# Kernel tuning notes

Measured on AMD Instinct MI355X. Metric: run time of the kernel, lower is better.

## Reference

```python
import jax, jax.numpy as jnp
import numpy as np

EPS = 1e-07


def _splat_single(frame, flow):
    # frame: [C, H, W], flow: [2, H, W] -> bilinear forward splatting (summation)
    C, H, W = frame.shape
    gx = jnp.arange(W, dtype=frame.dtype)[None, :]   # [1, W]
    gy = jnp.arange(H, dtype=frame.dtype)[:, None]   # [H, 1]
    tx = gx + flow[0]                                 # [H, W]
    ty = gy + flow[1]
    fx = jnp.floor(tx)
    fy = jnp.floor(ty)
    dx = tx - fx
    dy = ty - fy
    fx = fx.astype(jnp.int32)
    fy = fy.astype(jnp.int32)

    src = frame.reshape(C, H * W)                     # [C, HW]
    out = jnp.zeros((C, H * W), dtype=frame.dtype)
    # four bilinear corners: (x, y, weight)
    corners = [
        (fx,     fy,     (1.0 - dx) * (1.0 - dy)),
        (fx + 1, fy,     dx * (1.0 - dy)),
        (fx,     fy + 1, (1.0 - dx) * dy),
        (fx + 1, fy + 1, dx * dy),
    ]
    for cx, cy, w in corners:
        valid = (cx >= 0) & (cx < W) & (cy >= 0) & (cy < H)
        idx = jnp.where(valid, cy * W + cx, 0).reshape(-1)          # [HW]
        wv = jnp.where(valid, w, 0.0).reshape(1, -1)                # [1, HW]
        out = out.at[:, idx].add(src * wv)
    return out.reshape(C, H, W)


def _softmax_splat(frame, flow, importance_metric, eps=EPS):
    imp = jnp.exp(importance_metric)                  # [B,1,H,W]
    aug = jnp.concatenate([frame * imp, imp], axis=1) # [B,C+1,H,W]
    out = jax.vmap(_splat_single)(aug, flow)          # [B,C+1,H,W]
    return out[:, :-1] / (out[:, -1:] + eps)


def setup_inputs() -> dict:
    key = jax.random.key(0)
    k1, k2, k3 = jax.random.split(key, 3)
    B, C, H, W = 8, 4, 512, 960
    frame = jax.random.normal(k1, (B, C, H, W), dtype=jnp.float32)
    flow = jax.random.normal(k2, (B, 2, H, W), dtype=jnp.float32)
    importance_metric = jax.random.normal(k3, (B, 1, H, W), dtype=jnp.float32)
    return {"frame": frame, "flow": flow, "importance_metric": importance_metric}


def reference(frame, flow, importance_metric):
    return _softmax_splat(frame, flow, importance_metric)
```

## Files before the change

### kernel.cpp

```cpp
#include <hip/hip_runtime.h>
#include <hip/hip_fp16.h>
#include <math.h>


#define EPS 1e-7f

constexpr int B = 8, C = 4, H = 512, W = 960;
constexpr int HW = H * W;
constexpr int CHW = C * HW;
constexpr int NPIX = B * HW;

constexpr int TX = 32, TY = 32;
constexpr int RAD = 3;
constexpr int GROWS = 38;
constexpr int QX = 10;
constexpr int NQUAD = QX * GROWS;
constexpr int LSTRIDE = 41;
constexpr int NCELL = GROWS * LSTRIDE;

constexpr int NTILE_X = W / TX;
constexpr int NTILE = NTILE_X * (H / TY);
constexpr int BUCKET_CAP = 64;

struct alignas(8) HPack { __half2 a; __half2 b; };

__global__ __launch_bounds__(256) void outlier_pass(
    const float* __restrict__ frame,
    const float* __restrict__ flow,
    const float* __restrict__ imp,
    int* __restrict__ bcnt,
    float* __restrict__ bucket)
{
    int idx = blockIdx.x * blockDim.x + threadIdx.x;
    if (idx >= NPIX) return;
    int b = idx / HW;
    int p = idx - b * HW;
    int sy = p / W;
    int sx = p - sy * W;

    const size_t flb = (size_t)b * 2 * HW;
    float flx = flow[flb + p];
    float fly = flow[flb + HW + p];

    if (fabsf(flx) <= (float)(RAD - 1) && fabsf(fly) <= (float)(RAD - 1)) return;

    float tx = (float)sx + flx;
    float ty = (float)sy + fly;
    float fxf = floorf(tx);
    float fyf = floorf(ty);
    float dx = tx - fxf;
    float dy = ty - fyf;
    int fx = (int)fxf;
    int fy = (int)fyf;

    const size_t fb = (size_t)b * CHW;
    float im = __expf(imp[(size_t)b * HW + p]);
    float f0 = frame[fb + 0 * HW + p] * im;
    float f1 = frame[fb + 1 * HW + p] * im;
    float f2 = frame[fb + 2 * HW + p] * im;
    float f3 = frame[fb + 3 * HW + p] * im;

    #pragma unroll
    for (int cyi = 0; cyi < 2; ++cyi) {
        #pragma unroll
        for (int cxi = 0; cxi < 2; ++cxi) {
            int cx = fx + cxi;
            int cy = fy + cyi;
            if ((unsigned)cx >= (unsigned)W || (unsigned)cy >= (unsigned)H) continue;
            int ax = cx - sx; if (ax < 0) ax = -ax;
            int ay = cy - sy; if (ay < 0) ay = -ay;
            if (ax <= RAD && ay <= RAD) continue;
            float w = (cxi ? dx : 1.0f - dx) * (cyi ? dy : 1.0f - dy);
            int tile = b * NTILE + (cy >> 5) * NTILE_X + (cx >> 5);
            int e = atomicAdd(&bcnt[tile], 1);
            if (e < BUCKET_CAP) {
                float* ent = bucket + ((size_t)tile * BUCKET_CAP + e) * 8;
                ent[0] = __int_as_float((cy & 31) * TX + (cx & 31));
                ent[1] = f0 * w;
                ent[2] = f1 * w;
                ent[3] = f2 * w;
                ent[4] = f3 * w;
                ent[5] = im * w;
            }
        }
    }
}

__global__ __launch_bounds__(256) void splat_gather(
    const float* __restrict__ frame,
    const float* __restrict__ flow,
    const float* __restrict__ imp,
    float* __restrict__ out,
    const int* __restrict__ bcnt,
    const float* __restrict__ bucket)
{
    __shared__ float smem[5 * NCELL];
    float2* XY = (float2*)smem;
    float*  IM = smem + 2 * NCELL;
    HPack*  CH = (HPack*)(smem + 3 * NCELL);

    const int tid = threadIdx.x;
    const int x0 = blockIdx.x * TX;
    const int y0 = blockIdx.y * TY;
    const int b  = blockIdx.z;

    const float* fxp   = flow + (size_t)b * 2 * HW;
    const float* fyp   = fxp + HW;
    const float* imp_p = imp + (size_t)b * HW;
    const float* c0p   = frame + (size_t)b * CHW;
    const float* c1p   = c0p + HW;
    const float* c2p   = c1p + HW;
    const float* c3p   = c2p + HW;

    #pragma unroll
    for (int it = 0; it < 2; ++it) {
        int q = tid + it * 256;
        if (q < NQUAD) {
            int r = q / QX;
            int c = q - r * QX;
            int sy = y0 - RAD + r;
            int sx0 = x0 - 4 + 4 * c;
            int p = sy * W + sx0;
            int pc = p < 0 ? 0 : (p > HW - 4 ? HW - 4 : p);
            bool qv = ((unsigned)sy < (unsigned)H) & ((unsigned)sx0 < (unsigned)W);

            float4 vfx = *(const float4*)(fxp + pc);
            float4 vfy = *(const float4*)(fyp + pc);
            float4 vim = *(const float4*)(imp_p + pc);
            float4 v0  = *(const float4*)(c0p + pc);
            float4 v1  = *(const float4*)(c1p + pc);
            float4 v2  = *(const float4*)(c2p + pc);
            float4 v3  = *(const float4*)(c3p + pc);

            float aflx[4] = {vfx.x, vfx.y, vfx.z, vfx.w};
            float afly[4] = {vfy.x, vfy.y, vfy.z, vfy.w};
            float aim [4] = {vim.x, vim.y, vim.z, vim.w};
            float a0  [4] = {v0.x,  v0.y,  v0.z,  v0.w};
            float a1  [4] = {v1.x,  v1.y,  v1.z,  v1.w};
            float a2  [4] = {v2.x,  v2.y,  v2.z,  v2.w};
            float a3  [4] = {v3.x,  v3.y,  v3.z,  v3.w};

            int base = r * LSTRIDE + c * 4;
            #pragma unroll
            for (int k = 0; k < 4; ++k) {
                float im = qv ? __expf(aim[k]) : 0.0f;
                float txv = (float)(sx0 + k) + aflx[k];
                float tyv = (float)sy + afly[k];
                XY[base + k] = make_float2(txv, tyv);
                IM[base + k] = im;
                HPack hp;
                hp.a = __floats2half2_rn(a0[k] * im, a1[k] * im);
                hp.b = __floats2half2_rn(a2[k] * im, a3[k] * im);
                CH[base + k] = hp;
            }
        }
    }
    __syncthreads();

    const int oy    = tid & 31;
    const int strip = tid >> 5;
    const int oxl   = strip * 4;
    const float oxf0 = (float)(x0 + oxl);
    const float oyf  = (float)(y0 + oy);

    float accw[4] = {0.f, 0.f, 0.f, 0.f};
    float acc0[4] = {0.f, 0.f, 0.f, 0.f};
    float acc1[4] = {0.f, 0.f, 0.f, 0.f};
    float acc2[4] = {0.f, 0.f, 0.f, 0.f};
    float acc3[4] = {0.f, 0.f, 0.f, 0.f};

    for (int dyi = 0; dyi < 2 * RAD + 1; ++dyi) {
        int rowoff = (oy + dyi) * LSTRIDE + oxl;
        #pragma unroll
        for (int dxi = 1; dxi <= 10; ++dxi) {
            float2 xy = XY[rowoff + dxi];
            float wy = fmaxf(0.0f, 1.0f - fabsf(xy.y - oyf));
            if (wy > 0.0f) {
                float d0  = xy.x - oxf0;
                float wx0 = (dxi <= 7)              ? fmaxf(0.0f, 1.0f - fabsf(d0))        : 0.0f;
                float wx1 = (dxi >= 2 && dxi <= 8)  ? fmaxf(0.0f, 1.0f - fabsf(d0 - 1.0f)) : 0.0f;
                float wx2 = (dxi >= 3 && dxi <= 9)  ? fmaxf(0.0f, 1.0f - fabsf(d0 - 2.0f)) : 0.0f;
                float wx3 = (dxi >= 4)              ? fmaxf(0.0f, 1.0f - fabsf(d0 - 3.0f)) : 0.0f;
                float t0 = wx0 * wy, t1 = wx1 * wy, t2 = wx2 * wy, t3 = wx3 * wy;
                if ((t0 + t1) + (t2 + t3) > 0.0f) {
                    float im = IM[rowoff + dxi];
                    accw[0] = fmaf(im, t0, accw[0]);
                    accw[1] = fmaf(im, t1, accw[1]);
                    accw[2] = fmaf(im, t2, accw[2]);
                    accw[3] = fmaf(im, t3, accw[3]);
                    HPack hp = CH[rowoff + dxi];
                    float2 f01 = __half22float2(hp.a);
                    float2 f23 = __half22float2(hp.b);
                    acc0[0] = fmaf(f01.x, t0, acc0[0]);
                    acc0[1] = fmaf(f01.x, t1, acc0[1]);
                    acc0[2] = fmaf(f01.x, t2, acc0[2]);
                    acc0[3] = fmaf(f01.x, t3, acc0[3]);
                    acc1[0] = fmaf(f01.y, t0, acc1[0]);
                    acc1[1] = fmaf(f01.y, t1, acc1[1]);
                    acc1[2] = fmaf(f01.y, t2, acc1[2]);
                    acc1[3] = fmaf(f01.y, t3, acc1[3]);
                    acc2[0] = fmaf(f23.x, t0, acc2[0]);
                    acc2[1] = fmaf(f23.x, t1, acc2[1]);
                    acc2[2] = fmaf(f23.x, t2, acc2[2]);
                    acc2[3] = fmaf(f23.x, t3, acc2[3]);
                    acc3[0] = fmaf(f23.y, t0, acc3[0]);
                    acc3[1] = fmaf(f23.y, t1, acc3[1]);
                    acc3[2] = fmaf(f23.y, t2, acc3[2]);
                    acc3[3] = fmaf(f23.y, t3, acc3[3]);
                }
            }
        }
    }

    __syncthreads();
    const int tile = b * NTILE + blockIdx.y * NTILE_X + blockIdx.x;
    int cnt = bcnt[tile];
    if (cnt > BUCKET_CAP) cnt = BUCKET_CAP;
    if (cnt > 0) {
        float* oacc = smem;
        for (int i = tid; i < 5 * 1024; i += 256) oacc[i] = 0.0f;
        __syncthreads();
        const float* bb = bucket + (size_t)tile * BUCKET_CAP * 8;
        for (int e = tid; e < cnt; e += 256) {
            const float* ent = bb + (size_t)e * 8;
            int cell = __float_as_int(ent[0]);
            atomicAdd(&oacc[0 * 1024 + cell], ent[1]);
            atomicAdd(&oacc[1 * 1024 + cell], ent[2]);
            atomicAdd(&oacc[2 * 1024 + cell], ent[3]);
            atomicAdd(&oacc[3 * 1024 + cell], ent[4]);
            atomicAdd(&oacc[4 * 1024 + cell], ent[5]);
        }
        __syncthreads();
        int cell0 = oy * TX + oxl;
        #pragma unroll
        for (int j = 0; j < 4; ++j) {
            acc0[j] += oacc[0 * 1024 + cell0 + j];
            acc1[j] += oacc[1 * 1024 + cell0 + j];
            acc2[j] += oacc[2 * 1024 + cell0 + j];
            acc3[j] += oacc[3 * 1024 + cell0 + j];
            accw[j] += oacc[4 * 1024 + cell0 + j];
        }
    }

    float o0[4], o1[4], o2[4], o3[4];
    #pragma unroll
    for (int j = 0; j < 4; ++j) {
        float inv = 1.0f / (accw[j] + EPS);
        o0[j] = acc0[j] * inv;
        o1[j] = acc1[j] * inv;
        o2[j] = acc2[j] * inv;
        o3[j] = acc3[j] * inv;
    }
    size_t obase = (size_t)b * CHW + (size_t)(y0 + oy) * W + (x0 + oxl);
    *(float4*)(out + obase + 0 * HW) = make_float4(o0[0], o0[1], o0[2], o0[3]);
    *(float4*)(out + obase + 1 * HW) = make_float4(o1[0], o1[1], o1[2], o1[3]);
    *(float4*)(out + obase + 2 * HW) = make_float4(o2[0], o2[1], o2[2], o2[3]);
    *(float4*)(out + obase + 3 * HW) = make_float4(o3[0], o3[1], o3[2], o3[3]);
}

extern "C" void kernel_launch(void* const* d_in, const int* in_sizes, int n_in,
                              void* d_out, int out_size, void* d_ws, size_t ws_size,
                              hipStream_t stream) {
    const float* frame = (const float*)d_in[0];
    const float* flow  = (const float*)d_in[1];
    const float* imp   = (const float*)d_in[2];
    float* out = (float*)d_out;

    int*   bcnt   = (int*)d_ws;
    float* bucket = (float*)((char*)d_ws + 16384);

    hipMemsetAsync(bcnt, 0, B * NTILE * sizeof(int), stream);

    outlier_pass<<<(NPIX + 255) / 256, 256, 0, stream>>>(frame, flow, imp, bcnt, bucket);

    dim3 grid(W / TX, H / TY, B);
    splat_gather<<<grid, 256, 0, stream>>>(frame, flow, imp, out, bcnt, bucket);
}
```

Baseline: 117.8 us.

## Use 2x2 output quads in gather and vectorize outlier pass over four pixels

The gather kernel now has each thread own a 2x2 block of output pixels instead of a 1x4 strip. That shrinks the source window it scans from 7x10 to 8x8 candidates and computes two y-weights and two x-weights per candidate. The outlier pass processes four pixels per thread with float4 flow loads, cutting thread count and making its loads wider. Together these aim to reduce shared-memory reads and weight arithmetic in the hot gather loop. In exchange, output stores narrow from float4 to float2, and the outlier pass may see more branch divergence.

```diff
diff --git a/kernel.cpp b/kernel.cpp
--- a/kernel.cpp
+++ b/kernel.cpp
@@ -31,56 +31,69 @@
     int* __restrict__ bcnt,
     float* __restrict__ bucket)
 {
-    int idx = blockIdx.x * blockDim.x + threadIdx.x;
-    if (idx >= NPIX) return;
-    int b = idx / HW;
-    int p = idx - b * HW;
-    int sy = p / W;
-    int sx = p - sy * W;
+    int g = blockIdx.x * blockDim.x + threadIdx.x;
+    if (g >= NPIX / 4) return;
+    const int QHW = HW / 4;
+    int b = g / QHW;
+    int q = g - b * QHW;
+    int p0 = q * 4;
+    int sy = p0 / W;
+    int sx0 = p0 - sy * W;
 
     const size_t flb = (size_t)b * 2 * HW;
-    float flx = flow[flb + p];
-    float fly = flow[flb + HW + p];
-
-    if (fabsf(flx) <= (float)(RAD - 1) && fabsf(fly) <= (float)(RAD - 1)) return;
-
-    float tx = (float)sx + flx;
-    float ty = (float)sy + fly;
-    float fxf = floorf(tx);
-    float fyf = floorf(ty);
-    float dx = tx - fxf;
-    float dy = ty - fyf;
-    int fx = (int)fxf;
-    int fy = (int)fyf;
+    float4 vfx = *(const float4*)(flow + flb + p0);
+    float4 vfy = *(const float4*)(flow + flb + HW + p0);
+    float aflx[4] = {vfx.x, vfx.y, vfx.z, vfx.w};
+    float afly[4] = {vfy.x, vfy.y, vfy.z, vfy.w};
 
     const size_t fb = (size_t)b * CHW;
-    float im = __expf(imp[(size_t)b * HW + p]);
-    float f0 = frame[fb + 0 * HW + p] * im;
-    float f1 = frame[fb + 1 * HW + p] * im;
-    float f2 = frame[fb + 2 * HW + p] * im;
-    float f3 = frame[fb + 3 * HW + p] * im;
-
-    #pragma unroll
-    for (int cyi = 0; cyi < 2; ++cyi) {
+    const size_t ib = (size_t)b * HW;
+
+    #pragma unroll
+    for (int k = 0; k < 4; ++k) {
+        float flx = aflx[k];
+        float fly = afly[k];
+        if (fabsf(flx) <= (float)(RAD - 1) && fabsf(fly) <= (float)(RAD - 1)) continue;
+
+        int sx = sx0 + k;
+        int p = p0 + k;
+        float tx = (float)sx + flx;
+        float ty = (float)sy + fly;
+        float fxf = floorf(tx);
+        float fyf = floorf(ty);
+        float dx = tx - fxf;
+        float dy = ty - fyf;
+        int fx = (int)fxf;
+        int fy = (int)fyf;
+
+        float im = __expf(imp[ib + p]);
+        float f0 = frame[fb + 0 * HW + p] * im;
+        float f1 = frame[fb + 1 * HW + p] * im;
+        float f2 = frame[fb + 2 * HW + p] * im;
+        float f3 = frame[fb + 3 * HW + p] * im;
+
         #pragma unroll
-        for (int cxi = 0; cxi < 2; ++cxi) {
-            int cx = fx + cxi;
-            int cy = fy + cyi;
-            if ((unsigned)cx >= (unsigned)W || (unsigned)cy >= (unsigned)H) continue;
-            int ax = cx - sx; if (ax < 0) ax = -ax;
-            int ay = cy - sy; if (ay < 0) ay = -ay;
-            if (ax <= RAD && ay <= RAD) continue;
-            float w = (cxi ? dx : 1.0f - dx) * (cyi ? dy : 1.0f - dy);
-            int tile = b * NTILE + (cy >> 5) * NTILE_X + (cx >> 5);
-            int e = atomicAdd(&bcnt[tile], 1);
-            if (e < BUCKET_CAP) {
-                float* ent = bucket + ((size_t)tile * BUCKET_CAP + e) * 8;
-                ent[0] = __int_as_float((cy & 31) * TX + (cx & 31));
-                ent[1] = f0 * w;
-                ent[2] = f1 * w;
-                ent[3] = f2 * w;
-                ent[4] = f3 * w;
-                ent[5] = im * w;
+        for (int cyi = 0; cyi < 2; ++cyi) {
+            #pragma unroll
+            for (int cxi = 0; cxi < 2; ++cxi) {
+                int cx = fx + cxi;
+                int cy = fy + cyi;
+                if ((unsigned)cx >= (unsigned)W || (unsigned)cy >= (unsigned)H) continue;
+                int ax = cx - sx; if (ax < 0) ax = -ax;
+                int ay = cy - sy; if (ay < 0) ay = -ay;
+                if (ax <= RAD && ay <= RAD) continue;
+                float w = (cxi ? dx : 1.0f - dx) * (cyi ? dy : 1.0f - dy);
+                int tile = b * NTILE + (cy >> 5) * NTILE_X + (cx >> 5);
+                int e = atomicAdd(&bcnt[tile], 1);
+                if (e < BUCKET_CAP) {
+                    float* ent = bucket + ((size_t)tile * BUCKET_CAP + e) * 8;
+                    ent[0] = __int_as_float((cy & 31) * TX + (cx & 31));
+                    ent[1] = f0 * w;
+                    ent[2] = f1 * w;
+                    ent[3] = f2 * w;
+                    ent[4] = f3 * w;
+                    ent[5] = im * w;
+                }
             }
         }
     }
@@ -157,11 +170,10 @@
     }
     __syncthreads();
 
-    const int oy    = tid & 31;
-    const int strip = tid >> 5;
-    const int oxl   = strip * 4;
-    const float oxf0 = (float)(x0 + oxl);
-    const float oyf  = (float)(y0 + oy);
+    const int qx = tid & 15;
+    const int qy = tid >> 4;
+    const float ox0f = (float)(x0 + 2 * qx);
+    const float oy0f = (float)(y0 + 2 * qy);
 
     float accw[4] = {0.f, 0.f, 0.f, 0.f};
     float acc0[4] = {0.f, 0.f, 0.f, 0.f};
@@ -169,44 +181,45 @@
     float acc2[4] = {0.f, 0.f, 0.f, 0.f};
     float acc3[4] = {0.f, 0.f, 0.f, 0.f};
 
-    for (int dyi = 0; dyi < 2 * RAD + 1; ++dyi) {
-        int rowoff = (oy + dyi) * LSTRIDE + oxl;
+    for (int dyi = 0; dyi < 8; ++dyi) {
+        int rowoff = (2 * qy + dyi) * LSTRIDE + 2 * qx + 1;
         #pragma unroll
-        for (int dxi = 1; dxi <= 10; ++dxi) {
+        for (int dxi = 0; dxi < 8; ++dxi) {
             float2 xy = XY[rowoff + dxi];
-            float wy = fmaxf(0.0f, 1.0f - fabsf(xy.y - oyf));
-            if (wy > 0.0f) {
-                float d0  = xy.x - oxf0;
-                float wx0 = (dxi <= 7)              ? fmaxf(0.0f, 1.0f - fabsf(d0))        : 0.0f;
-                float wx1 = (dxi >= 2 && dxi <= 8)  ? fmaxf(0.0f, 1.0f - fabsf(d0 - 1.0f)) : 0.0f;
-                float wx2 = (dxi >= 3 && dxi <= 9)  ? fmaxf(0.0f, 1.0f - fabsf(d0 - 2.0f)) : 0.0f;
-                float wx3 = (dxi >= 4)              ? fmaxf(0.0f, 1.0f - fabsf(d0 - 3.0f)) : 0.0f;
-                float t0 = wx0 * wy, t1 = wx1 * wy, t2 = wx2 * wy, t3 = wx3 * wy;
-                if ((t0 + t1) + (t2 + t3) > 0.0f) {
+            float ddy = xy.y - oy0f;
+            float wy0 = (dyi <= 6) ? fmaxf(0.0f, 1.0f - fabsf(ddy))        : 0.0f;
+            float wy1 = (dyi >= 1) ? fmaxf(0.0f, 1.0f - fabsf(ddy - 1.0f)) : 0.0f;
+            if (wy0 + wy1 > 0.0f) {
+                float ddx = xy.x - ox0f;
+                float wx0 = (dxi <= 6) ? fmaxf(0.0f, 1.0f - fabsf(ddx))        : 0.0f;
+                float wx1 = (dxi >= 1) ? fmaxf(0.0f, 1.0f - fabsf(ddx - 1.0f)) : 0.0f;
+                float t00 = wy0 * wx0, t01 = wy0 * wx1;
+                float t10 = wy1 * wx0, t11 = wy1 * wx1;
+                if ((t00 + t01) + (t10 + t11) > 0.0f) {
                     float im = IM[rowoff + dxi];
-                    accw[0] = fmaf(im, t0, accw[0]);
-                    accw[1] = fmaf(im, t1, accw[1]);
-                    accw[2] = fmaf(im, t2, accw[2]);
-                    accw[3] = fmaf(im, t3, accw[3]);
                     HPack hp = CH[rowoff + dxi];
                     float2 f01 = __half22float2(hp.a);
                     float2 f23 = __half22float2(hp.b);
-                    acc0[0] = fmaf(f01.x, t0, acc0[0]);
-                    acc0[1] = fmaf(f01.x, t1, acc0[1]);
-                    acc0[2] = fmaf(f01.x, t2, acc0[2]);
-                    acc0[3] = fmaf(f01.x, t3, acc0[3]);
-                    acc1[0] = fmaf(f01.y, t0, acc1[0]);
-                    acc1[1] = fmaf(f01.y, t1, acc1[1]);
-                    acc1[2] = fmaf(f01.y, t2, acc1[2]);
-                    acc1[3] = fmaf(f01.y, t3, acc1[3]);
-                    acc2[0] = fmaf(f23.x, t0, acc2[0]);
-                    acc2[1] = fmaf(f23.x, t1, acc2[1]);
-                    acc2[2] = fmaf(f23.x, t2, acc2[2]);
-                    acc2[3] = fmaf(f23.x, t3, acc2[3]);
-                    acc3[0] = fmaf(f23.y, t0, acc3[0]);
-                    acc3[1] = fmaf(f23.y, t1, acc3[1]);
-                    acc3[2] = fmaf(f23.y, t2, acc3[2]);
-                    acc3[3] = fmaf(f23.y, t3, acc3[3]);
+                    accw[0] = fmaf(im, t00, accw[0]);
+                    accw[1] = fmaf(im, t01, accw[1]);
+                    accw[2] = fmaf(im, t10, accw[2]);
+                    accw[3] = fmaf(im, t11, accw[3]);
+                    acc0[0] = fmaf(f01.x, t00, acc0[0]);
+                    acc0[1] = fmaf(f01.x, t01, acc0[1]);
+                    acc0[2] = fmaf(f01.x, t10, acc0[2]);
+                    acc0[3] = fmaf(f01.x, t11, acc0[3]);
+                    acc1[0] = fmaf(f01.y, t00, acc1[0]);
+                    acc1[1] = fmaf(f01.y, t01, acc1[1]);
+                    acc1[2] = fmaf(f01.y, t10, acc1[2]);
+                    acc1[3] = fmaf(f01.y, t11, acc1[3]);
+                    acc2[0] = fmaf(f23.x, t00, acc2[0]);
+                    acc2[1] = fmaf(f23.x, t01, acc2[1]);
+                    acc2[2] = fmaf(f23.x, t10, acc2[2]);
+                    acc2[3] = fmaf(f23.x, t11, acc2[3]);
+                    acc3[0] = fmaf(f23.y, t00, acc3[0]);
+                    acc3[1] = fmaf(f23.y, t01, acc3[1]);
+                    acc3[2] = fmaf(f23.y, t10, acc3[2]);
+                    acc3[3] = fmaf(f23.y, t11, acc3[3]);
                 }
             }
         }
@@ -231,31 +244,34 @@
             atomicAdd(&oacc[4 * 1024 + cell], ent[5]);
         }
         __syncthreads();
-        int cell0 = oy * TX + oxl;
         #pragma unroll
-        for (int j = 0; j < 4; ++j) {
-            acc0[j] += oacc[0 * 1024 + cell0 + j];
-            acc1[j] += oacc[1 * 1024 + cell0 + j];
-            acc2[j] += oacc[2 * 1024 + cell0 + j];
-            acc3[j] += oacc[3 * 1024 + cell0 + j];
-            accw[j] += oacc[4 * 1024 + cell0 + j];
-        }
-    }
-
-    float o0[4], o1[4], o2[4], o3[4];
-    #pragma unroll
-    for (int j = 0; j < 4; ++j) {
-        float inv = 1.0f / (accw[j] + EPS);
-        o0[j] = acc0[j] * inv;
-        o1[j] = acc1[j] * inv;
-        o2[j] = acc2[j] * inv;
-        o3[j] = acc3[j] * inv;
-    }
-    size_t obase = (size_t)b * CHW + (size_t)(y0 + oy) * W + (x0 + oxl);
-    *(float4*)(out + obase + 0 * HW) = make_float4(o0[0], o0[1], o0[2], o0[3]);
-    *(float4*)(out + obase + 1 * HW) = make_float4(o1[0], o1[1], o1[2], o1[3]);
-    *(float4*)(out + obase + 2 * HW) = make_float4(o2[0], o2[1], o2[2], o2[3]);
-    *(float4*)(out + obase + 3 * HW) = make_float4(o3[0], o3[1], o3[2], o3[3]);
+        for (int k = 0; k < 2; ++k) {
+            #pragma unroll
+            for (int j = 0; j < 2; ++j) {
+                int cell = (2 * qy + k) * TX + 2 * qx + j;
+                int a = k * 2 + j;
+                acc0[a] += oacc[0 * 1024 + cell];
+                acc1[a] += oacc[1 * 1024 + cell];
+                acc2[a] += oacc[2 * 1024 + cell];
+                acc3[a] += oacc[3 * 1024 + cell];
+                accw[a] += oacc[4 * 1024 + cell];
+            }
+        }
+    }
+
+    float inv[4];
+    #pragma unroll
+    for (int a = 0; a < 4; ++a) inv[a] = 1.0f / (accw[a] + EPS);
+
+    #pragma unroll
+    for (int k = 0; k < 2; ++k) {
+        size_t obase = (size_t)b * CHW + (size_t)(y0 + 2 * qy + k) * W + (x0 + 2 * qx);
+        int a0i = k * 2, a1i = k * 2 + 1;
+        *(float2*)(out + obase + 0 * HW) = make_float2(acc0[a0i] * inv[a0i], acc0[a1i] * inv[a1i]);
+        *(float2*)(out + obase + 1 * HW) = make_float2(acc1[a0i] * inv[a0i], acc1[a1i] * inv[a1i]);
+        *(float2*)(out + obase + 2 * HW) = make_float2(acc2[a0i] * inv[a0i], acc2[a1i] * inv[a1i]);
+        *(float2*)(out + obase + 3 * HW) = make_float2(acc3[a0i] * inv[a0i], acc3[a1i] * inv[a1i]);
+    }
 }
 
 extern "C" void kernel_launch(void* const* d_in, const int* in_sizes, int n_in,
@@ -271,7 +287,7 @@
 
     hipMemsetAsync(bcnt, 0, B * NTILE * sizeof(int), stream);
 
-    outlier_pass<<<(NPIX + 255) / 256, 256, 0, stream>>>(frame, flow, imp, bcnt, bucket);
+    outlier_pass<<<(NPIX / 4 + 255) / 256, 256, 0, stream>>>(frame, flow, imp, bcnt, bucket);
 
     dim3 grid(W / TX, H / TY, B);
     splat_gather<<<grid, 256, 0, stream>>>(frame, flow, imp, out, bcnt, bucket);
```

After: 109.1 us. -7.4%, faster.
